# Kernel optimization log

Measured on AMD Instinct MI355X. Metric: run time of the kernel, lower is better.

The kernel has to match this reference:

```python
import jax, jax.numpy as jnp
import numpy as np

# Config constants (match init_kwargs)
E = 32          # num_experts
K = 4           # num_experts_per_token
G = 4           # num_expert_group
TG = 2          # topk_group
H = 2048        # hidden_size
F = 1024        # moe_intermediate_size
FS = 2048       # shared expert intermediate (moe_intermediate_size * num_shared_experts)
SCALE = 2.0     # routed_scaling_factor
B, S = 2, 1024
N = B * S
CAP = 2 * (N * K // E)


def setup_inputs() -> dict:
    key = jax.random.key(0)
    ks = jax.random.split(key, 9)
    w = 0.02  # init scale for weights
    return {
        "hidden_states": jax.random.normal(ks[0], (B, S, H), jnp.float32),
        "gate_w": jax.random.normal(ks[1], (E, H), jnp.float32) * w,
        "gate_bias": jax.random.normal(ks[2], (E,), jnp.float32) * w,
        "w1": jax.random.normal(ks[3], (E, H, F), jnp.float32) * w,
        "w2": jax.random.normal(ks[4], (E, F, H), jnp.float32) * w,
        "w3": jax.random.normal(ks[5], (E, H, F), jnp.float32) * w,
        "shared_gate": jax.random.normal(ks[6], (H, FS), jnp.float32) * w,
        "shared_up": jax.random.normal(ks[7], (H, FS), jnp.float32) * w,
        "shared_down": jax.random.normal(ks[8], (FS, H), jnp.float32) * w,
    }


def _gate(x, gate_w, gate_bias):
    # x: [N, H] -> (topk_idx [N,K] int32, topk_w [N,K] f32)
    logits = x @ gate_w.T                       # [N, E]
    scores = jax.nn.sigmoid(logits)
    sc = scores + gate_bias                     # scores_for_choice
    n = x.shape[0]
    grp = sc.reshape(n, G, E // G)
    group_scores = jax.lax.top_k(grp, 2)[0].sum(-1)          # [N, G]
    _, gidx = jax.lax.top_k(group_scores, TG)                # [N, TG]
    gmask = jnp.zeros((n, G), sc.dtype).at[jnp.arange(n)[:, None], gidx].set(1.0)
    smask = jnp.repeat(gmask, E // G, axis=1)                # [N, E]
    tmp = jnp.where(smask > 0, sc, 0.0)
    _, topk_idx = jax.lax.top_k(tmp, K)                      # [N, K]
    topk_w = jnp.take_along_axis(scores, topk_idx, axis=1)
    topk_w = topk_w / (topk_w.sum(-1, keepdims=True) + 1e-20)  # renormalize (K>1)
    return topk_idx, topk_w * SCALE


def _moe(x, topk_idx, topk_w, w1, w2, w3):
    # Capacity-based dispatch -> grouped SwiGLU GEMMs -> weighted combine.
    n = x.shape[0]
    flat_e = topk_idx.reshape(-1)                            # [N*K]
    oh = jax.nn.one_hot(flat_e, E, dtype=jnp.int32)
    pos = (jnp.cumsum(oh, axis=0) * oh).sum(-1) - 1          # slot within expert
    keep = pos < CAP
    slot = jnp.where(keep, pos, CAP)                         # CAP -> dropped via mode='drop'
    x_rep = jnp.repeat(x, K, axis=0)                         # [N*K, H]
    buf = jnp.zeros((E, CAP, H), x.dtype).at[flat_e, slot].set(x_rep, mode='drop')
    h = jax.nn.silu(jnp.einsum('ech,ehf->ecf', buf, w1)) * jnp.einsum('ech,ehf->ecf', buf, w3)
    ob = jnp.einsum('ecf,efh->ech', h, w2)                   # [E, CAP, H]
    y = ob[flat_e, jnp.minimum(slot, CAP - 1)]               # [N*K, H]
    y = jnp.where(keep[:, None], y, 0.0)
    return (y.reshape(n, K, H) * topk_w[:, :, None]).sum(1)  # [N, H]


def reference(hidden_states, gate_w, gate_bias, w1, w2, w3, shared_gate, shared_up, shared_down):
    b, s, h = hidden_states.shape
    x = hidden_states.reshape(-1, h)
    topk_idx, topk_w = _gate(x, gate_w, gate_bias)
    out = _moe(x, topk_idx, topk_w, w1, w2, w3)
    shared = (jax.nn.silu(x @ shared_gate) * (x @ shared_up)) @ shared_down
    return (out + shared).reshape(b, s, h)
```

## Files before the change

### kernel.cpp

```cpp
#include <hip/hip_runtime.h>
#include <stdint.h>
#include <math.h>

#define NTOK 2048
#define HDIM 2048
#define FDIM 1024
#define NEXP 32
#define TOPK 4
#define NGRP 4
#define CAP  512

typedef _Float16 f16;
typedef _Float16 half8 __attribute__((ext_vector_type(8)));
typedef _Float16 half2v __attribute__((ext_vector_type(2)));
typedef float f32x4 __attribute__((ext_vector_type(4)));

__device__ __forceinline__ int swz3(int n) { return (n ^ (n >> 2)) & 3; }

__global__ __launch_bounds__(256) void gateconv_kernel(const float* __restrict__ x,
                                                       const float* __restrict__ gw,
                                                       const float* __restrict__ gb,
                                                       int* __restrict__ tidx,
                                                       float* __restrict__ tw,
                                                       f16* __restrict__ xbt) {
  int t = blockIdx.x;
  int tid = threadIdx.x;
  int e = tid >> 3, p = tid & 7;
  const f32x4* xr = (const f32x4*)(x + (size_t)t * HDIM);
  const f32x4* wr = (const f32x4*)(gw + (size_t)e * HDIM);
  float s = 0.f;
  for (int c = 0; c < 64; c++) {
    f32x4 a = xr[p + c * 8], w = wr[p + c * 8];
    s += a[0] * w[0] + a[1] * w[1] + a[2] * w[2] + a[3] * w[3];
  }
  s += __shfl_down(s, 4, 8);
  s += __shfl_down(s, 2, 8);
  s += __shfl_down(s, 1, 8);
  __shared__ float lg[NEXP];
  if (p == 0) lg[e] = s;

  {
    int c8 = tid * 8;
    const float* pp = x + (size_t)t * HDIM + c8;
    f32x4 a = *(const f32x4*)pp;
    f32x4 b = *(const f32x4*)(pp + 4);
    half8 v;
    v[0] = (f16)a[0]; v[1] = (f16)a[1]; v[2] = (f16)a[2]; v[3] = (f16)a[3];
    v[4] = (f16)b[0]; v[5] = (f16)b[1]; v[6] = (f16)b[2]; v[7] = (f16)b[3];
    *(half8*)((char*)xbt + (size_t)(c8 >> 5) * 131072 + t * 64 + (c8 & 31) * 2) = v;
  }

  __syncthreads();
  if (tid == 0) {
    float sc[NEXP], scb[NEXP];
    for (int i = 0; i < NEXP; i++) {
      sc[i] = 1.f / (1.f + expf(-lg[i]));
      scb[i] = sc[i] + gb[i];
    }
    float gs[NGRP];
    for (int g = 0; g < NGRP; g++) {
      float m1 = -1e30f, m2 = -1e30f;
      for (int j = 0; j < 8; j++) {
        float v = scb[g * 8 + j];
        if (v > m1) { m2 = m1; m1 = v; }
        else if (v > m2) m2 = v;
      }
      gs[g] = m1 + m2;
    }
    int g1 = 0; float bv = gs[0];
    for (int g = 1; g < NGRP; g++) if (gs[g] > bv) { bv = gs[g]; g1 = g; }
    int g2 = -1; bv = -1e30f;
    for (int g = 0; g < NGRP; g++) if (g != g1 && gs[g] > bv) { bv = gs[g]; g2 = g; }
    float cand[NEXP];
    for (int i = 0; i < NEXP; i++) {
      int g = i >> 3;
      cand[i] = (g == g1 || g == g2) ? scb[i] : 0.0f;
    }
    int isel[TOPK]; float wsel[TOPK]; float wsum = 0.f;
    bool used[NEXP] = {};
    for (int k = 0; k < TOPK; k++) {
      int best = 0; float bw = -1e30f;
      for (int i = 0; i < NEXP; i++)
        if (!used[i] && cand[i] > bw) { bw = cand[i]; best = i; }
      used[best] = true;
      isel[k] = best;
      wsel[k] = sc[best];
      wsum += wsel[k];
    }
    float inv = 2.0f / (wsum + 1e-20f);
    for (int k = 0; k < TOPK; k++) {
      tidx[t * TOPK + k] = isel[k];
      tw[t * TOPK + k] = wsel[k] * inv;
    }
  }
}

__global__ __launch_bounds__(256) void dispatch_kernel(const int* __restrict__ tidx,
                                                       const float* __restrict__ tw,
                                                       int* __restrict__ tok,
                                                       float* __restrict__ wt,
                                                       int* __restrict__ cnt) {
  int e = blockIdx.x, tid = threadIdx.x, wv = tid >> 6, lane = tid & 63;
  __shared__ int wsum[4];
  __shared__ int sbase;
  if (tid == 0) sbase = 0;
  __syncthreads();
  for (int c = 0; c < (NTOK * TOPK) / 256; c++) {
    int i = c * 256 + tid;
    int fe = tidx[i];
    bool flag = (fe == e);
    unsigned long long b = __ballot(flag ? 1 : 0);
    int lr = __popcll(b & ((1ull << lane) - 1ull));
    if (lane == 0) wsum[wv] = __popcll(b);
    __syncthreads();
    int off = 0;
    for (int w2 = 0; w2 < wv; w2++) off += wsum[w2];
    int tot = wsum[0] + wsum[1] + wsum[2] + wsum[3];
    int base = sbase;
    if (flag) {
      int pos = base + off + lr;
      if (pos < CAP) {
        tok[e * CAP + pos] = i >> 2;
        wt[e * CAP + pos] = tw[i];
      }
    }
    __syncthreads();
    if (tid == 0) sbase = base + tot;
  }
  __syncthreads();
  if (tid == 0) cnt[e] = min(sbase, CAP);
}

__global__ void scan_kernel(const int* __restrict__ cnt, int* __restrict__ offs) {
  if (threadIdx.x == 0) {
    int s = 0;
    for (int e = 0; e < NEXP; e++) { offs[e] = s; s += cnt[e]; }
  }
}

__global__ __launch_bounds__(256) void gather_kernel(const f16* __restrict__ xbt,
                                                     const int* __restrict__ tok,
                                                     const int* __restrict__ cnt,
                                                     const int* __restrict__ offs,
                                                     f16* __restrict__ xg) {
  int bid = blockIdx.x;
  int t = bid & 63, e = bid >> 6;
  int cn = cnt[e];
  int tid = threadIdx.x;
  char* dst = (char*)xg + (size_t)offs[e] * 4096 + (size_t)t * cn * 64;
  const char* srcb = (const char*)xbt + (size_t)t * 131072;
  for (int s = tid; s < cn; s += 256) {
    const uint4* sp = (const uint4*)(srcb + (size_t)tok[e * CAP + s] * 64);
    uint4 v0 = sp[0], v1 = sp[1], v2 = sp[2], v3 = sp[3];
    uint4* dp = (uint4*)(dst + s * 64);
    dp[0] = v0; dp[1] = v1; dp[2] = v2; dp[3] = v3;
  }
}

#define SYNC() { asm volatile("s_waitcnt lgkmcnt(0)" ::: "memory"); __builtin_amdgcn_s_barrier(); }

__device__ __forceinline__ void core128(const char* __restrict__ Ab, int tsA, int NKt,
                                        const float* __restrict__ Bb, int ND,
                                        char* lds, f32x4 (&acc)[4][4]) {
  int tid = threadIdx.x, lane = tid & 63, wv = tid >> 6;
  int wn = (wv & 1) * 64;
  int wm = (wv >> 1) * 64;
  int kg = 2 * (lane >> 4) + 8 * wv;
  int n4 = 4 * (lane & 15);
  const float* Br0 = Bb + (size_t)kg * ND + n4;
  const float* Br1 = Bb + (size_t)(kg + 1) * ND + n4;

  unsigned aoff[4];
#pragma unroll
  for (int mf = 0; mf < 4; mf++)
    aoff[mf] = (wm + mf * 16 + (lane & 15)) * 64 + ((lane >> 4) << 4);

  int wo[8];
#pragma unroll
  for (int h = 0; h < 2; h++)
#pragma unroll
    for (int q = 0; q < 4; q++) {
      int n = n4 + 64 * h + q;
      wo[h * 4 + q] = n * 64 + (((kg >> 3) ^ swz3(n)) << 4) + (kg & 7) * 2;
    }

  half8 afA[4], afB[4], bf[4];
  f32x4 E0, E1, E2, E3, O0, O1, O2, O3;

#define LOADB(tt, S0, S1, S2, S3) { size_t _o = (size_t)(tt) * 32 * ND; \
    S0 = *(const f32x4*)(Br0 + _o);      S1 = *(const f32x4*)(Br1 + _o); \
    S2 = *(const f32x4*)(Br0 + _o + 64); S3 = *(const f32x4*)(Br1 + _o + 64); }

#define WRITEB(S0, S1, S2, S3, par) { char* _b = lds + (par) * 8192; \
    _Pragma("unroll") for (int _q = 0; _q < 4; _q++) { \
      half2v _h; _h[0] = (f16)S0[_q]; _h[1] = (f16)S1[_q]; \
      *(half2v*)(_b + wo[_q]) = _h; } \
    _Pragma("unroll") for (int _q = 0; _q < 4; _q++) { \
      half2v _h; _h[0] = (f16)S2[_q]; _h[1] = (f16)S3[_q]; \
      *(half2v*)(_b + wo[4 + _q]) = _h; } }

#define BFREAD(par) { _Pragma("unroll") for (int _f = 0; _f < 4; _f++) { \
      int _n = wn + _f * 16 + (lane & 15); \
      bf[_f] = *(const half8*)(lds + (par) * 8192 + _n * 64 + (((lane >> 4) ^ swz3(_n)) << 4)); } }

#define LOADA(tt, AF) { _Pragma("unroll") for (int _m = 0; _m < 4; _m++) \
      AF[_m] = *(const half8*)(Ab + (size_t)(tt) * tsA + aoff[_m]); }

#define DOMFMA(AF) { _Pragma("unroll") for (int _m = 0; _m < 4; _m++) \
      _Pragma("unroll") for (int _f = 0; _f < 4; _f++) \
        acc[_m][_f] = __builtin_amdgcn_mfma_f32_16x16x32_f16(AF[_m], bf[_f], acc[_m][_f], 0, 0, 0); }

  LOADB(0, E0, E1, E2, E3)
  LOADB(1, O0, O1, O2, O3)
  WRITEB(E0, E1, E2, E3, 0)
  LOADA(0, afA)
  SYNC()

  for (int t = 0; t < NKt; t += 2) {
    BFREAD(0)
    LOADA(t + 1, afB)
    WRITEB(O0, O1, O2, O3, 1)
    if (t + 2 < NKt) LOADB(t + 2, E0, E1, E2, E3)
    DOMFMA(afA)
    SYNC()
    BFREAD(1)
    if (t + 2 < NKt) {
      LOADA(t + 2, afA)
      WRITEB(E0, E1, E2, E3, 0)
      if (t + 3 < NKt) LOADB(t + 3, O0, O1, O2, O3)
    }
    DOMFMA(afB)
    if (t + 2 < NKt) SYNC()
  }

#undef LOADB
#undef WRITEB
#undef BFREAD
#undef LOADA
#undef DOMFMA
}

__global__ __launch_bounds__(256, 2) void fused_up_kernel(
    const f16* __restrict__ xg, const f16* __restrict__ xbt,
    const float* __restrict__ w1, const float* __restrict__ w3,
    const float* __restrict__ sg, const float* __restrict__ su,
    f16* __restrict__ hg, f16* __restrict__ hu,
    f16* __restrict__ hsg, f16* __restrict__ hsu,
    const int* __restrict__ cnt, const int* __restrict__ offs) {
  __shared__ __align__(16) char lds[16384];
  int bid = blockIdx.x;
  int tid = threadIdx.x, lane = tid & 63, wv = tid >> 6;
  int wm = (wv >> 1) * 64, wn = (wv & 1) * 64, koff = (lane >> 4) << 2;

  f32x4 acc[4][4];
#pragma unroll
  for (int mf = 0; mf < 4; mf++)
#pragma unroll
    for (int nf = 0; nf < 4; nf++) acc[mf][nf] = (f32x4){0.f, 0.f, 0.f, 0.f};

  if (bid < 2048) {
    int elo = bid & 7, n = (bid >> 3) & 7, m = (bid >> 6) & 3, ehi = (bid >> 8) & 3, mat = bid >> 10;
    int e = elo + ehi * 8;
    int ce = cnt[e];
    int m0 = m * 128;
    if (m0 >= ce) return;
    int oe = offs[e];
    const char* Ab = (const char*)xg + (size_t)oe * 4096 + m0 * 64;
    const float* B = (mat ? w3 : w1) + (size_t)e * 2048 * 1024 + n * 128;
    core128(Ab, ce * 64, 64, B, 1024, lds, acc);
    char* Hb = (char*)(mat ? hu : hg) + (size_t)oe * 2048;
    size_t kts = (size_t)ce * 64;
#pragma unroll
    for (int mf = 0; mf < 4; mf++)
#pragma unroll
      for (int j = 0; j < 4; j++) {
        int gs = m0 + wm + mf * 16 + koff + j;
        if (gs < ce) {
#pragma unroll
          for (int nf = 0; nf < 4; nf++) {
            int gc = n * 128 + wn + nf * 16 + (lane & 15);
            *(f16*)(Hb + (size_t)(gc >> 5) * kts + gs * 64 + (gc & 31) * 2) = (f16)acc[mf][nf][j];
          }
        }
      }
  } else {
    int b2 = bid - 2048;
    int mat = b2 >> 8, rem = b2 & 255, m = rem >> 4, n = rem & 15;
    int m0 = m * 128;
    const char* Ab = (const char*)xbt + m0 * 64;
    const float* B = (mat ? su : sg) + n * 128;
    core128(Ab, 131072, 64, B, 2048, lds, acc);
    char* Hb = (char*)(mat ? hsu : hsg);
#pragma unroll
    for (int mf = 0; mf < 4; mf++)
#pragma unroll
      for (int j = 0; j < 4; j++) {
        int gs = m0 + wm + mf * 16 + koff + j;
#pragma unroll
        for (int nf = 0; nf < 4; nf++) {
          int gc = n * 128 + wn + nf * 16 + (lane & 15);
          *(f16*)(Hb + (size_t)(gc >> 5) * 131072 + gs * 64 + (gc & 31) * 2) = (f16)acc[mf][nf][j];
        }
      }
  }
}

__global__ __launch_bounds__(256) void combine_kernel(
    const f16* __restrict__ hg, const f16* __restrict__ hu, f16* __restrict__ hbuf,
    const f16* __restrict__ hsg, const f16* __restrict__ hsu, f16* __restrict__ hs) {
  size_t i = ((size_t)blockIdx.x * 256 + threadIdx.x) * 8;
  const f16 *gp, *up;
  f16* op;
  if (i < 8388608) { gp = hg + i; up = hu + i; op = hbuf + i; }
  else { size_t j = i - 8388608; gp = hsg + j; up = hsu + j; op = hs + j; }
  half8 g = *(const half8*)gp;
  half8 u = *(const half8*)up;
  half8 o;
#pragma unroll
  for (int k = 0; k < 8; k++) {
    float gv = (float)g[k];
    float uv = (float)u[k];
    o[k] = (f16)(gv / (1.f + expf(-gv)) * uv);
  }
  *(half8*)op = o;
}

__global__ __launch_bounds__(256, 2) void fused_down_kernel(
    const f16* __restrict__ hbuf, const f16* __restrict__ hs,
    const float* __restrict__ w2, const float* __restrict__ sd,
    float* __restrict__ out, const int* __restrict__ tok,
    const float* __restrict__ wt, const int* __restrict__ cnt,
    const int* __restrict__ offs) {
  __shared__ __align__(16) char lds[16384];
  int bid = blockIdx.x;
  int tid = threadIdx.x, lane = tid & 63, wv = tid >> 6;
  int wm = (wv >> 1) * 64, wn = (wv & 1) * 64, koff = (lane >> 4) << 2;

  f32x4 acc[4][4];
#pragma unroll
  for (int mf = 0; mf < 4; mf++)
#pragma unroll
    for (int nf = 0; nf < 4; nf++) acc[mf][nf] = (f32x4){0.f, 0.f, 0.f, 0.f};

  if (bid < 2048) {
    int elo = bid & 7, n = (bid >> 3) & 15, m = (bid >> 7) & 3, ehi = (bid >> 9) & 3;
    int e = elo + ehi * 8;
    int ce = cnt[e];
    int m0 = m * 128;
    if (m0 >= ce) return;
    int oe = offs[e];
    const char* Ab = (const char*)hbuf + (size_t)oe * 2048 + m0 * 64;
    const float* B = w2 + (size_t)e * 1024 * 2048 + n * 128;
    core128(Ab, ce * 64, 32, B, 2048, lds, acc);
    const int* tokp = tok + e * CAP;
    const float* wtp = wt + e * CAP;
#pragma unroll
    for (int mf = 0; mf < 4; mf++)
#pragma unroll
      for (int j = 0; j < 4; j++) {
        int gs = m0 + wm + mf * 16 + koff + j;
        if (gs < ce) {
          int tk = tokp[gs];
          float w = wtp[gs];
#pragma unroll
          for (int nf = 0; nf < 4; nf++) {
            int gc = n * 128 + wn + nf * 16 + (lane & 15);
            atomicAdd(out + (size_t)tk * HDIM + gc, acc[mf][nf][j] * w);
          }
        }
      }
  } else {
    int b2 = bid - 2048;
    int m = b2 >> 4, n = b2 & 15;
    int m0 = m * 128;
    const char* Ab = (const char*)hs + m0 * 64;
    const float* B = sd + n * 128;
    core128(Ab, 131072, 64, B, 2048, lds, acc);
#pragma unroll
    for (int mf = 0; mf < 4; mf++)
#pragma unroll
      for (int j = 0; j < 4; j++) {
        int gs = m0 + wm + mf * 16 + koff + j;
#pragma unroll
        for (int nf = 0; nf < 4; nf++) {
          int gc = n * 128 + wn + nf * 16 + (lane & 15);
          atomicAdd(out + (size_t)gs * HDIM + gc, acc[mf][nf][j]);
        }
      }
  }
}

extern "C" void kernel_launch(void* const* d_in, const int* in_sizes, int n_in,
                              void* d_out, int out_size, void* d_ws, size_t ws_size,
                              hipStream_t stream) {
  const float* x  = (const float*)d_in[0];
  const float* gw = (const float*)d_in[1];
  const float* gb = (const float*)d_in[2];
  const float* w1 = (const float*)d_in[3];
  const float* w2 = (const float*)d_in[4];
  const float* w3 = (const float*)d_in[5];
  const float* sg = (const float*)d_in[6];
  const float* su = (const float*)d_in[7];
  const float* sd = (const float*)d_in[8];
  float* out = (float*)d_out;
  char* ws = (char*)d_ws;

  f16*   xbt  = (f16*)(ws);
  f16*   hsg  = (f16*)(ws + 8388608);
  f16*   hsu  = (f16*)(ws + 16777216);
  f16*   hs   = (f16*)(ws + 25165824);
  f16*   hg   = (f16*)(ws + 33554432);
  f16*   hu   = (f16*)(ws + 50331648);
  f16*   xg   = (f16*)(ws + 67108864);
  f16*   hbuf = (f16*)(ws + 67108864);
  int*   tok  = (int*)(ws + 101711872);
  float* wt   = (float*)(ws + 101777408);
  int*   tidx = (int*)(ws + 101842944);
  float* tw   = (float*)(ws + 101875712);
  int*   cnt  = (int*)(ws + 101908480);
  int*   offs = (int*)(ws + 101908608);

  gateconv_kernel<<<2048, 256, 0, stream>>>(x, gw, gb, tidx, tw, xbt);
  dispatch_kernel<<<32, 256, 0, stream>>>(tidx, tw, tok, wt, cnt);
  scan_kernel<<<1, 32, 0, stream>>>(cnt, offs);
  gather_kernel<<<2048, 256, 0, stream>>>(xbt, tok, cnt, offs, xg);

  fused_up_kernel<<<2560, 256, 0, stream>>>(xg, xbt, w1, w3, sg, su,
                                            hg, hu, hsg, hsu, cnt, offs);
  combine_kernel<<<6144, 256, 0, stream>>>(hg, hu, hbuf, hsg, hsu, hs);

  hipMemsetAsync(out, 0, (size_t)out_size * sizeof(float), stream);
  fused_down_kernel<<<2304, 256, 0, stream>>>(hbuf, hs, w2, sd, out, tok, wt, cnt, offs);
}
```

Before: 518.8 us.

## Double the GEMM K-tile to 64 with wider LDS swizzle, halving barriers

The shared 128x128 GEMM core now stages 64 K-values per iteration instead of 32. It loads eight B vectors per thread and keeps two K-subtiles of A fragments in registers. The LDS row stride doubles to 128 bytes with an 8-way XOR swizzle, and LDS per block grows to 32 KB. All callers halve their K-tile count. This halves the number of barrier syncs and outer iterations per K sweep, at the cost of more registers and LDS, which may reduce occupancy.

```diff
diff --git a/kernel.cpp b/kernel.cpp
--- a/kernel.cpp
+++ b/kernel.cpp
@@ -14,8 +14,6 @@
 typedef _Float16 half8 __attribute__((ext_vector_type(8)));
 typedef _Float16 half2v __attribute__((ext_vector_type(2)));
 typedef float f32x4 __attribute__((ext_vector_type(4)));
-
-__device__ __forceinline__ int swz3(int n) { return (n ^ (n >> 2)) & 3; }
 
 __global__ __launch_bounds__(256) void gateconv_kernel(const float* __restrict__ x,
                                                        const float* __restrict__ gw,
@@ -175,62 +173,84 @@
   for (int mf = 0; mf < 4; mf++)
     aoff[mf] = (wm + mf * 16 + (lane & 15)) * 64 + ((lane >> 4) << 4);
 
-  int wo[8];
-#pragma unroll
-  for (int h = 0; h < 2; h++)
-#pragma unroll
-    for (int q = 0; q < 4; q++) {
-      int n = n4 + 64 * h + q;
-      wo[h * 4 + q] = n * 64 + (((kg >> 3) ^ swz3(n)) << 4) + (kg & 7) * 2;
-    }
-
-  half8 afA[4], afB[4], bf[4];
-  f32x4 E0, E1, E2, E3, O0, O1, O2, O3;
-
-#define LOADB(tt, S0, S1, S2, S3) { size_t _o = (size_t)(tt) * 32 * ND; \
+  int wo[2][2][4];
+#pragma unroll
+  for (int hi = 0; hi < 2; hi++)
+#pragma unroll
+    for (int h = 0; h < 2; h++)
+#pragma unroll
+      for (int q = 0; q < 4; q++) {
+        int n = n4 + 64 * h + q;
+        int c = (kg >> 3) + 4 * hi;
+        wo[hi][h][q] = n * 128 + ((c ^ (n & 7)) << 4) + (kg & 7) * 2;
+      }
+
+  half8 af[8], bf[4];
+  f32x4 E0, E1, E2, E3, E4, E5, E6, E7;
+  f32x4 O0, O1, O2, O3, O4, O5, O6, O7;
+
+#define LOADB(tt, S0,S1,S2,S3,S4,S5,S6,S7) { size_t _o = (size_t)(tt) * 64 * ND; \
+    size_t _u = _o + (size_t)32 * ND; \
     S0 = *(const f32x4*)(Br0 + _o);      S1 = *(const f32x4*)(Br1 + _o); \
-    S2 = *(const f32x4*)(Br0 + _o + 64); S3 = *(const f32x4*)(Br1 + _o + 64); }
-
-#define WRITEB(S0, S1, S2, S3, par) { char* _b = lds + (par) * 8192; \
+    S2 = *(const f32x4*)(Br0 + _o + 64); S3 = *(const f32x4*)(Br1 + _o + 64); \
+    S4 = *(const f32x4*)(Br0 + _u);      S5 = *(const f32x4*)(Br1 + _u); \
+    S6 = *(const f32x4*)(Br0 + _u + 64); S7 = *(const f32x4*)(Br1 + _u + 64); }
+
+#define WRITEB(S0,S1,S2,S3,S4,S5,S6,S7, par) { char* _b = lds + (par) * 16384; \
     _Pragma("unroll") for (int _q = 0; _q < 4; _q++) { \
       half2v _h; _h[0] = (f16)S0[_q]; _h[1] = (f16)S1[_q]; \
-      *(half2v*)(_b + wo[_q]) = _h; } \
+      *(half2v*)(_b + wo[0][0][_q]) = _h; } \
     _Pragma("unroll") for (int _q = 0; _q < 4; _q++) { \
       half2v _h; _h[0] = (f16)S2[_q]; _h[1] = (f16)S3[_q]; \
-      *(half2v*)(_b + wo[4 + _q]) = _h; } }
-
-#define BFREAD(par) { _Pragma("unroll") for (int _f = 0; _f < 4; _f++) { \
+      *(half2v*)(_b + wo[0][1][_q]) = _h; } \
+    _Pragma("unroll") for (int _q = 0; _q < 4; _q++) { \
+      half2v _h; _h[0] = (f16)S4[_q]; _h[1] = (f16)S5[_q]; \
+      *(half2v*)(_b + wo[1][0][_q]) = _h; } \
+    _Pragma("unroll") for (int _q = 0; _q < 4; _q++) { \
+      half2v _h; _h[0] = (f16)S6[_q]; _h[1] = (f16)S7[_q]; \
+      *(half2v*)(_b + wo[1][1][_q]) = _h; } }
+
+#define BFREAD(par, kk) { _Pragma("unroll") for (int _f = 0; _f < 4; _f++) { \
       int _n = wn + _f * 16 + (lane & 15); \
-      bf[_f] = *(const half8*)(lds + (par) * 8192 + _n * 64 + (((lane >> 4) ^ swz3(_n)) << 4)); } }
-
-#define LOADA(tt, AF) { _Pragma("unroll") for (int _m = 0; _m < 4; _m++) \
-      AF[_m] = *(const half8*)(Ab + (size_t)(tt) * tsA + aoff[_m]); }
-
-#define DOMFMA(AF) { _Pragma("unroll") for (int _m = 0; _m < 4; _m++) \
+      int _c = (kk) * 4 + (lane >> 4); \
+      bf[_f] = *(const half8*)(lds + (par) * 16384 + _n * 128 + ((_c ^ (_n & 7)) << 4)); } }
+
+#define LOADA(tt) { _Pragma("unroll") for (int _m = 0; _m < 4; _m++) \
+      af[_m] = *(const half8*)(Ab + (size_t)(2 * (tt)) * tsA + aoff[_m]); \
+    _Pragma("unroll") for (int _m = 0; _m < 4; _m++) \
+      af[4 + _m] = *(const half8*)(Ab + (size_t)(2 * (tt) + 1) * tsA + aoff[_m]); }
+
+#define DOMFMA(base) { _Pragma("unroll") for (int _m = 0; _m < 4; _m++) \
       _Pragma("unroll") for (int _f = 0; _f < 4; _f++) \
-        acc[_m][_f] = __builtin_amdgcn_mfma_f32_16x16x32_f16(AF[_m], bf[_f], acc[_m][_f], 0, 0, 0); }
-
-  LOADB(0, E0, E1, E2, E3)
-  LOADB(1, O0, O1, O2, O3)
-  WRITEB(E0, E1, E2, E3, 0)
-  LOADA(0, afA)
+        acc[_m][_f] = __builtin_amdgcn_mfma_f32_16x16x32_f16(af[(base) + _m], bf[_f], acc[_m][_f], 0, 0, 0); }
+
+  LOADB(0, E0,E1,E2,E3,E4,E5,E6,E7)
+  LOADB(1, O0,O1,O2,O3,O4,O5,O6,O7)
+  WRITEB(E0,E1,E2,E3,E4,E5,E6,E7, 0)
+  LOADA(0)
   SYNC()
 
   for (int t = 0; t < NKt; t += 2) {
-    BFREAD(0)
-    LOADA(t + 1, afB)
-    WRITEB(O0, O1, O2, O3, 1)
-    if (t + 2 < NKt) LOADB(t + 2, E0, E1, E2, E3)
-    DOMFMA(afA)
+    BFREAD(0, 0)
+    WRITEB(O0,O1,O2,O3,O4,O5,O6,O7, 1)
+    if (t + 2 < NKt) LOADB(t + 2, E0,E1,E2,E3,E4,E5,E6,E7)
+    DOMFMA(0)
+    BFREAD(0, 1)
+    DOMFMA(4)
+    LOADA(t + 1)
     SYNC()
-    BFREAD(1)
+    BFREAD(1, 0)
     if (t + 2 < NKt) {
-      LOADA(t + 2, afA)
-      WRITEB(E0, E1, E2, E3, 0)
-      if (t + 3 < NKt) LOADB(t + 3, O0, O1, O2, O3)
-    }
-    DOMFMA(afB)
-    if (t + 2 < NKt) SYNC()
+      WRITEB(E0,E1,E2,E3,E4,E5,E6,E7, 0)
+      if (t + 3 < NKt) LOADB(t + 3, O0,O1,O2,O3,O4,O5,O6,O7)
+    }
+    DOMFMA(0)
+    BFREAD(1, 1)
+    DOMFMA(4)
+    if (t + 2 < NKt) {
+      LOADA(t + 2)
+      SYNC()
+    }
   }
 
 #undef LOADB
@@ -247,7 +267,7 @@
     f16* __restrict__ hg, f16* __restrict__ hu,
     f16* __restrict__ hsg, f16* __restrict__ hsu,
     const int* __restrict__ cnt, const int* __restrict__ offs) {
-  __shared__ __align__(16) char lds[16384];
+  __shared__ __align__(16) char lds[32768];
   int bid = blockIdx.x;
   int tid = threadIdx.x, lane = tid & 63, wv = tid >> 6;
   int wm = (wv >> 1) * 64, wn = (wv & 1) * 64, koff = (lane >> 4) << 2;
@@ -267,7 +287,7 @@
     int oe = offs[e];
     const char* Ab = (const char*)xg + (size_t)oe * 4096 + m0 * 64;
     const float* B = (mat ? w3 : w1) + (size_t)e * 2048 * 1024 + n * 128;
-    core128(Ab, ce * 64, 64, B, 1024, lds, acc);
+    core128(Ab, ce * 64, 32, B, 1024, lds, acc);
     char* Hb = (char*)(mat ? hu : hg) + (size_t)oe * 2048;
     size_t kts = (size_t)ce * 64;
 #pragma unroll
@@ -289,7 +309,7 @@
     int m0 = m * 128;
     const char* Ab = (const char*)xbt + m0 * 64;
     const float* B = (mat ? su : sg) + n * 128;
-    core128(Ab, 131072, 64, B, 2048, lds, acc);
+    core128(Ab, 131072, 32, B, 2048, lds, acc);
     char* Hb = (char*)(mat ? hsu : hsg);
 #pragma unroll
     for (int mf = 0; mf < 4; mf++)
@@ -331,7 +351,7 @@
     float* __restrict__ out, const int* __restrict__ tok,
     const float* __restrict__ wt, const int* __restrict__ cnt,
     const int* __restrict__ offs) {
-  __shared__ __align__(16) char lds[16384];
+  __shared__ __align__(16) char lds[32768];
   int bid = blockIdx.x;
   int tid = threadIdx.x, lane = tid & 63, wv = tid >> 6;
   int wm = (wv >> 1) * 64, wn = (wv & 1) * 64, koff = (lane >> 4) << 2;
@@ -351,7 +371,7 @@
     int oe = offs[e];
     const char* Ab = (const char*)hbuf + (size_t)oe * 2048 + m0 * 64;
     const float* B = w2 + (size_t)e * 1024 * 2048 + n * 128;
-    core128(Ab, ce * 64, 32, B, 2048, lds, acc);
+    core128(Ab, ce * 64, 16, B, 2048, lds, acc);
     const int* tokp = tok + e * CAP;
     const float* wtp = wt + e * CAP;
 #pragma unroll
@@ -375,7 +395,7 @@
     int m0 = m * 128;
     const char* Ab = (const char*)hs + m0 * 64;
     const float* B = sd + n * 128;
-    core128(Ab, 131072, 64, B, 2048, lds, acc);
+    core128(Ab, 131072, 32, B, 2048, lds, acc);
 #pragma unroll
     for (int mf = 0; mf < 4; mf++)
 #pragma unroll
```

Measured after the change: 530.4 us. +2.2%, slower.
